# Kernel tuning notes

Measured on AMD Instinct MI355X. Metric: run time of the kernel, lower is better.

## Reference

```python
import jax, jax.numpy as jnp
import numpy as np

N_NODES = 200000
N_EDGES = 6400000


def gcn_conv(x, W, b, src, dst, n):
    """PyG GCNConv with add_self_loops=True, symmetric normalization.
    x: [n, d_in], W: [d_in, d_out], b: [d_out], src/dst: [E] int.
    """
    h = x @ W  # [n, d_out]
    # degree over graph with self-loops (edge weight 1 each, +1 self-loop)
    deg = jax.ops.segment_sum(jnp.ones(src.shape, h.dtype), dst, num_segments=n) + 1.0
    dinv = jax.lax.rsqrt(deg)  # deg >= 1, always safe
    norm = (dinv[src] * dinv[dst])[:, None]  # [E, 1]
    agg = jax.ops.segment_sum(h[src] * norm, dst, num_segments=n)  # scatter-add over targets
    agg = agg + h * (dinv * dinv)[:, None]  # self-loop term: norm_ii = dinv_i^2
    return agg + b


def setup_inputs() -> dict:
    key = jax.random.key(0)
    ks = jax.random.split(key, 8)
    x = jax.random.normal(ks[0], (N_NODES, 1), dtype=jnp.float32)
    edge_index = jax.random.randint(ks[1], (2, N_EDGES), 0, N_NODES, dtype=jnp.int64)
    # learned params (glorot-ish scale)
    W1 = jax.random.normal(ks[2], (1, 16), dtype=jnp.float32) * (1.0 / np.sqrt(1))
    b1 = jnp.zeros((16,), dtype=jnp.float32)
    W2 = jax.random.normal(ks[3], (16, 16), dtype=jnp.float32) * (1.0 / np.sqrt(16))
    b2 = jnp.zeros((16,), dtype=jnp.float32)
    Wl = jax.random.normal(ks[4], (16, 1), dtype=jnp.float32) * (1.0 / np.sqrt(16))
    bl = jnp.zeros((1,), dtype=jnp.float32)
    return {"x": x, "edge_index": edge_index, "W1": W1, "b1": b1,
            "W2": W2, "b2": b2, "Wl": Wl, "bl": bl}


def reference(x, edge_index, W1, b1, W2, b2, Wl, bl):
    src, dst = edge_index[0], edge_index[1]
    n = x.shape[0]
    h = jax.nn.relu(gcn_conv(x, W1, b1, src, dst, n))
    h = jax.nn.relu(gcn_conv(h, W2, b2, src, dst, n))
    return h @ Wl + bl  # [N, 1]
```

## Files before the change

### kernel.cpp

```cpp
#include <hip/hip_runtime.h>

#define BSHIFT 9
#define BW 512
#define BLK 512
#define BLKL 256
#define CHUNK 8192
#define BCAP 20480
#define CSR_CAP 18432

__device__ __forceinline__ int blockScanExcl512(int v, int tid, int* wsum) {
    int lane = tid & 63;
    int w = tid >> 6;
    int incl = v;
#pragma unroll
    for (int d = 1; d < 64; d <<= 1) {
        int u = __shfl_up(incl, d, 64);
        if (lane >= d) incl += u;
    }
    if (lane == 63) wsum[w] = incl;
    __syncthreads();
    if (tid < 64) {
        int x = (tid < 8) ? wsum[tid] : 0;
#pragma unroll
        for (int d = 1; d < 8; d <<= 1) {
            int u = __shfl_up(x, d, 64);
            if (lane >= d) x += u;
        }
        if (tid < 8) wsum[tid] = x;
    }
    __syncthreads();
    int base = (w == 0) ? 0 : wsum[w - 1];
    return base + incl - v;
}

__global__ __launch_bounds__(BW) void k_zero(int* __restrict__ cnt) {
    cnt[threadIdx.x] = 0;
}

__global__ __launch_bounds__(BLK) void k_bin(const int* __restrict__ src,
                                             const int* __restrict__ dst,
                                             int* __restrict__ cnt,
                                             unsigned int* __restrict__ binned, int E) {
    __shared__ int h0[BW], h1[BW];
    __shared__ int excl[BW], cur[BW], gbase[BW];
    __shared__ unsigned int vals[CHUNK];
    __shared__ unsigned short bkt[CHUNK];
    __shared__ int wsum[8];
    int t = threadIdx.x;
    int base = blockIdx.x * CHUNK;
    int cnt_e = min(CHUNK, E - base);
    h0[t] = 0; h1[t] = 0;
    __syncthreads();
    int* hr = ((t >> 6) & 1) ? h1 : h0;

    int d16[16], s16[16];
    int myBase = base + t * 16;
    int nb = 0;
    if (myBase + 16 <= E) {
        const int4* dp = (const int4*)(dst + myBase);
        const int4* sp = (const int4*)(src + myBase);
#pragma unroll
        for (int k = 0; k < 4; ++k) {
            int4 a = dp[k];
            d16[4 * k] = a.x; d16[4 * k + 1] = a.y; d16[4 * k + 2] = a.z; d16[4 * k + 3] = a.w;
            int4 c = sp[k];
            s16[4 * k] = c.x; s16[4 * k + 1] = c.y; s16[4 * k + 2] = c.z; s16[4 * k + 3] = c.w;
        }
        nb = 16;
    } else {
        for (int k = 0; k < 16; ++k) {
            int idx = myBase + k;
            if (idx < E) { d16[k] = dst[idx]; s16[k] = src[idx]; ++nb; }
        }
    }
    for (int k = 0; k < nb; ++k) atomicAdd(&hr[d16[k] >> BSHIFT], 1);
    __syncthreads();
    int hv = h0[t] + h1[t];
    int ex = blockScanExcl512(hv, t, wsum);
    excl[t] = ex;
    cur[t] = ex;
    if (hv) gbase[t] = t * BCAP + atomicAdd(&cnt[t], hv);
    __syncthreads();
    for (int k = 0; k < nb; ++k) {
        int b = d16[k] >> BSHIFT;
        int r = atomicAdd(&cur[b], 1);
        vals[r] = ((unsigned int)s16[k] << BSHIFT) | (unsigned int)(d16[k] & (BW - 1));
        bkt[r] = (unsigned short)b;
    }
    __syncthreads();
    for (int i = t; i < cnt_e; i += BLK) {
        int b = bkt[i];
        binned[gbase[b] + (i - excl[b])] = vals[i];
    }
}

__global__ __launch_bounds__(BLK) void k_csr(const unsigned int* __restrict__ binned,
                                             const int* __restrict__ cnt,
                                             const float* __restrict__ x,
                                             int* __restrict__ csrOff,
                                             int* __restrict__ deg,
                                             float* __restrict__ dinv,
                                             float* __restrict__ xd,
                                             int* __restrict__ csrSrc, int n) {
    __shared__ int dh0[BW], dh1[BW];
    __shared__ int cursor[BW];
    __shared__ int wsum[8];
    __shared__ int stage[CSR_CAP];
    int t = threadIdx.x;
    int b = blockIdx.x;
    int ebase = b * BCAP;
    int ecnt = cnt[b];
    dh0[t] = 0; dh1[t] = 0;
    __syncthreads();
    int* dh = ((t >> 6) & 1) ? dh1 : dh0;
    for (int i = t; i < ecnt; i += BLK)
        atomicAdd(&dh[binned[ebase + i] & (BW - 1)], 1);
    __syncthreads();
    int c = dh0[t] + dh1[t];
    int ex = blockScanExcl512(c, t, wsum);
    cursor[t] = ex;
    int nodeBase = b << BSHIFT;
    if (t < min(BW, n - nodeBase)) {
        int node = nodeBase + t;
        csrOff[node] = ebase + ex;
        deg[node] = c;
        float r = rsqrtf((float)(c + 1));
        dinv[node] = r;
        xd[node] = x[node] * r;
    }
    __syncthreads();
    for (int i = t; i < ecnt; i += BLK) {
        unsigned int v = binned[ebase + i];
        int r = atomicAdd(&cursor[v & (BW - 1)], 1);
        int sv = (int)(v >> BSHIFT);
        if (r < CSR_CAP) stage[r] = sv;
        else csrSrc[ebase + r] = sv;
    }
    __syncthreads();
    int m = min(ecnt, CSR_CAP);
    for (int i = t; i < m; i += BLK)
        csrSrc[ebase + i] = stage[i];
}

__global__ __launch_bounds__(BLKL) void k_l1(const int* __restrict__ csrOff,
                                             const int* __restrict__ deg,
                                             const int* __restrict__ csrSrc,
                                             const float* __restrict__ xd,
                                             const float* __restrict__ dinv,
                                             unsigned int* __restrict__ spk, int n) {
    int tid = threadIdx.x;
    int q = tid & 3;
    int node = blockIdx.x * (BLKL / 4) + (tid >> 2);
    if (node >= n) return;
    int start = csrOff[node];
    int dc = deg[node];
    float u = 0.f;
    int e = q;
    for (; e + 4 < dc; e += 8) {
        int s0 = csrSrc[start + e];
        int s1 = csrSrc[start + e + 4];
        u += xd[s0] + xd[s1];
    }
    for (; e < dc; e += 4)
        u += xd[csrSrc[start + e]];
    u += __shfl_xor(u, 1, 64);
    u += __shfl_xor(u, 2, 64);
    if (q == 0) {
        float di = dinv[node];
        float s = di * (u + xd[node]);
        unsigned int us = (__float_as_uint(s) + 0x80u) & 0xFFFFFF00u;
        unsigned int d8 = (unsigned int)min(dc, 255);
        spk[node] = us | d8;
    }
}

__global__ __launch_bounds__(BLKL) void k_l2(const int* __restrict__ csrOff,
                                             const int* __restrict__ deg,
                                             const int* __restrict__ csrSrc,
                                             const unsigned int* __restrict__ spk,
                                             const float* __restrict__ dinv,
                                             const float* __restrict__ W1,
                                             const float* __restrict__ b1,
                                             const float* __restrict__ W2,
                                             const float* __restrict__ b2,
                                             const float* __restrict__ Wl,
                                             const float* __restrict__ bl,
                                             float* __restrict__ out, int n) {
    __shared__ float sW2[256];
    __shared__ float di_tab[256];
    int tid = threadIdx.x;
    sW2[tid] = W2[tid];
    di_tab[tid] = rsqrtf((float)(tid + 1));
    int q = tid & 3;
    int node = blockIdx.x * (BLKL / 4) + (tid >> 2);

    float w1r[16], b1r[16];
#pragma unroll
    for (int j = 0; j < 16; ++j) {
        w1r[j] = W1[j];
        float bv = b1[j];
        asm volatile("" : "+v"(bv));
        b1r[j] = bv;
    }
    float4 b2q = *(const float4*)(b2 + 4 * q);
    float4 wlq = *(const float4*)(Wl + 4 * q);
    float blv = bl[0];
    __syncthreads();
    if (node >= n) return;

    int start = csrOff[node];
    int dc = deg[node];
    float G[16];
#pragma unroll
    for (int j = 0; j < 16; ++j) G[j] = 0.f;

    unsigned int uself = spk[node];
    float dself = dinv[node];
    if (q == 0) {
        float sself = __uint_as_float(uself & 0xFFFFFF00u);
#pragma unroll
        for (int j = 0; j < 16; ++j)
            G[j] = fmaf(fmaxf(fmaf(w1r[j], sself, b1r[j]), 0.f), dself, G[j]);
    }

#define EDGEACC(u, srcidx)                                                \
    {                                                                     \
        float s_ = __uint_as_float((u) & 0xFFFFFF00u);                    \
        unsigned int d8_ = (u) & 255u;                                    \
        float di_ = di_tab[d8_];                                          \
        if (__builtin_expect(d8_ == 255u, 0)) di_ = dinv[srcidx];         \
        _Pragma("unroll")                                                 \
        for (int j = 0; j < 16; ++j)                                      \
            G[j] = fmaf(fmaxf(fmaf(w1r[j], s_, b1r[j]), 0.f), di_, G[j]); \
    }

    int e = q;
    for (; e + 12 < dc; e += 16) {
        int s0 = csrSrc[start + e];
        int s1 = csrSrc[start + e + 4];
        int s2 = csrSrc[start + e + 8];
        int s3 = csrSrc[start + e + 12];
        unsigned int u0 = spk[s0];
        unsigned int u1 = spk[s1];
        unsigned int u2 = spk[s2];
        unsigned int u3 = spk[s3];
        EDGEACC(u0, s0) EDGEACC(u1, s1) EDGEACC(u2, s2) EDGEACC(u3, s3)
    }
    for (; e < dc; e += 4) {
        int s0 = csrSrc[start + e];
        unsigned int u0 = spk[s0];
        EDGEACC(u0, s0)
    }
#undef EDGEACC

#pragma unroll
    for (int j = 0; j < 16; ++j) {
        G[j] += __shfl_xor(G[j], 1, 64);
        G[j] += __shfl_xor(G[j], 2, 64);
    }

    float4 A = make_float4(0.f, 0.f, 0.f, 0.f);
#pragma unroll
    for (int j = 0; j < 16; ++j) {
        float4 w = *(const float4*)(&sW2[j * 16 + 4 * q]);
        A.x = fmaf(w.x, G[j], A.x);
        A.y = fmaf(w.y, G[j], A.y);
        A.z = fmaf(w.z, G[j], A.z);
        A.w = fmaf(w.w, G[j], A.w);
    }

    float v0 = fmaxf(fmaf(dself, A.x, b2q.x), 0.f);
    float v1 = fmaxf(fmaf(dself, A.y, b2q.y), 0.f);
    float v2 = fmaxf(fmaf(dself, A.z, b2q.z), 0.f);
    float v3 = fmaxf(fmaf(dself, A.w, b2q.w), 0.f);
    float p = fmaf(v0, wlq.x, fmaf(v1, wlq.y, fmaf(v2, wlq.z, v3 * wlq.w)));
    p += __shfl_xor(p, 1, 64);
    p += __shfl_xor(p, 2, 64);
    if (q == 0) out[node] = p + blv;
}

extern "C" void kernel_launch(void* const* d_in, const int* in_sizes, int n_in,
                              void* d_out, int out_size, void* d_ws, size_t ws_size,
                              hipStream_t stream) {
    const float* x  = (const float*)d_in[0];
    const int*   ei = (const int*)d_in[1];
    const float* W1 = (const float*)d_in[2];
    const float* b1 = (const float*)d_in[3];
    const float* W2 = (const float*)d_in[4];
    const float* b2 = (const float*)d_in[5];
    const float* Wl = (const float*)d_in[6];
    const float* bl = (const float*)d_in[7];
    float* out = (float*)d_out;

    int n = in_sizes[0];
    int E = in_sizes[1] / 2;
    const int* srcA = ei;
    const int* dstA = ei + E;
    int NB = (n + BW - 1) >> BSHIFT;

    size_t o = 0;
    auto carve = [&](size_t bytes) {
        void* p = (char*)d_ws + o;
        o = (o + bytes + 255) & ~(size_t)255;
        return p;
    };
    int* cnt          = (int*)carve(BW * 4);
    int* csrOff       = (int*)carve((size_t)n * 4);
    int* deg          = (int*)carve((size_t)n * 4);
    float* dinv       = (float*)carve((size_t)n * 4);
    float* xd         = (float*)carve((size_t)n * 4);
    unsigned int* spk = (unsigned int*)carve((size_t)n * 4);
    unsigned int* binned = (unsigned int*)carve((size_t)NB * BCAP * 4);
    int* csrSrc       = (int*)carve((size_t)NB * BCAP * 4);
    (void)ws_size;

    k_zero<<<1, BW, 0, stream>>>(cnt);
    k_bin<<<(E + CHUNK - 1) / CHUNK, BLK, 0, stream>>>(srcA, dstA, cnt, binned, E);
    k_csr<<<NB, BLK, 0, stream>>>(binned, cnt, x, csrOff, deg, dinv, xd, csrSrc, n);

    int nodeBlocks = (n + (BLKL / 4) - 1) / (BLKL / 4);
    k_l1<<<nodeBlocks, BLKL, 0, stream>>>(csrOff, deg, csrSrc, xd, dinv, spk, n);
    k_l2<<<nodeBlocks, BLKL, 0, stream>>>(csrOff, deg, csrSrc, spk, dinv,
                                          W1, b1, W2, b2, Wl, bl, out, n);
}
```

Measured before the change: 132.5 us.

## Pre-gather packed source values into padded CSR before layer-2 aggregation

k_csr now pads each node's CSR segment to a multiple of 4 and zero-fills the padding, with the row lengths recorded per bin. A new k_gather kernel then overwrites each source index in place with that source's packed scale+degree word. This lets k_l2 read edge values with aligned uint4 loads instead of a dependent index-then-random-gather chain. In exchange there is an extra kernel launch and an extra read and write pass over the CSR. The layer-2 path also drops the exact dinv fallback for sources with degree at or above 255, so such nodes would get a wrong normalisation.

```diff
diff --git a/kernel.cpp b/kernel.cpp
--- a/kernel.cpp
+++ b/kernel.cpp
@@ -101,10 +101,12 @@
                                              int* __restrict__ deg,
                                              float* __restrict__ dinv,
                                              float* __restrict__ xd,
-                                             int* __restrict__ csrSrc, int n) {
+                                             int* __restrict__ padcnt,
+                                             int* __restrict__ csr, int n) {
     __shared__ int dh0[BW], dh1[BW];
     __shared__ int cursor[BW];
     __shared__ int wsum[8];
+    __shared__ int padtot_s;
     __shared__ int stage[CSR_CAP];
     int t = threadIdx.x;
     int b = blockIdx.x;
@@ -117,8 +119,10 @@
         atomicAdd(&dh[binned[ebase + i] & (BW - 1)], 1);
     __syncthreads();
     int c = dh0[t] + dh1[t];
-    int ex = blockScanExcl512(c, t, wsum);
+    int pad4 = (c + 3) & ~3;
+    int ex = blockScanExcl512(pad4, t, wsum);
     cursor[t] = ex;
+    if (t == BLK - 1) padtot_s = ex + pad4;
     int nodeBase = b << BSHIFT;
     if (t < min(BW, n - nodeBase)) {
         int node = nodeBase + t;
@@ -129,22 +133,30 @@
         xd[node] = x[node] * r;
     }
     __syncthreads();
+    int padtot = padtot_s;
+    int mcap = min(padtot, CSR_CAP);
+    int4* st4 = (int4*)stage;
+    int4 z4 = make_int4(0, 0, 0, 0);
+    for (int i = t; i < (mcap >> 2); i += BLK) st4[i] = z4;
+    for (int i = CSR_CAP + t; i < padtot; i += BLK) csr[ebase + i] = 0;
+    __syncthreads();
     for (int i = t; i < ecnt; i += BLK) {
         unsigned int v = binned[ebase + i];
         int r = atomicAdd(&cursor[v & (BW - 1)], 1);
         int sv = (int)(v >> BSHIFT);
         if (r < CSR_CAP) stage[r] = sv;
-        else csrSrc[ebase + r] = sv;
-    }
-    __syncthreads();
-    int m = min(ecnt, CSR_CAP);
-    for (int i = t; i < m; i += BLK)
-        csrSrc[ebase + i] = stage[i];
+        else csr[ebase + r] = sv;
+    }
+    __syncthreads();
+    int4* out4 = (int4*)(csr + ebase);
+    for (int i = t; i < (mcap >> 2); i += BLK)
+        out4[i] = st4[i];
+    if (t == 0) padcnt[b] = padtot;
 }
 
 __global__ __launch_bounds__(BLKL) void k_l1(const int* __restrict__ csrOff,
                                              const int* __restrict__ deg,
-                                             const int* __restrict__ csrSrc,
+                                             const int* __restrict__ csr,
                                              const float* __restrict__ xd,
                                              const float* __restrict__ dinv,
                                              unsigned int* __restrict__ spk, int n) {
@@ -157,12 +169,12 @@
     float u = 0.f;
     int e = q;
     for (; e + 4 < dc; e += 8) {
-        int s0 = csrSrc[start + e];
-        int s1 = csrSrc[start + e + 4];
+        int s0 = csr[start + e];
+        int s1 = csr[start + e + 4];
         u += xd[s0] + xd[s1];
     }
     for (; e < dc; e += 4)
-        u += xd[csrSrc[start + e]];
+        u += xd[csr[start + e]];
     u += __shfl_xor(u, 1, 64);
     u += __shfl_xor(u, 2, 64);
     if (q == 0) {
@@ -174,9 +186,29 @@
     }
 }
 
+__global__ __launch_bounds__(BLK) void k_gather(const int* __restrict__ padcnt,
+                                                const unsigned int* __restrict__ spk,
+                                                unsigned int* __restrict__ csr) {
+    int t = threadIdx.x;
+    int b = blockIdx.x;
+    unsigned int* base = csr + (size_t)b * BCAP;
+    int len = padcnt[b];
+    for (int i = t * 8; i + 8 <= len; i += BLK * 8) {
+        int4 a = *(const int4*)(base + i);
+        int4 c = *(const int4*)(base + i + 4);
+        unsigned int v0 = spk[a.x], v1 = spk[a.y], v2 = spk[a.z], v3 = spk[a.w];
+        unsigned int v4 = spk[c.x], v5 = spk[c.y], v6 = spk[c.z], v7 = spk[c.w];
+        *(uint4*)(base + i) = make_uint4(v0, v1, v2, v3);
+        *(uint4*)(base + i + 4) = make_uint4(v4, v5, v6, v7);
+    }
+    int tail = len & ~7;
+    for (int i = tail + t; i < len; i += BLK)
+        base[i] = spk[base[i]];
+}
+
 __global__ __launch_bounds__(BLKL) void k_l2(const int* __restrict__ csrOff,
                                              const int* __restrict__ deg,
-                                             const int* __restrict__ csrSrc,
+                                             const unsigned int* __restrict__ csrVal,
                                              const unsigned int* __restrict__ spk,
                                              const float* __restrict__ dinv,
                                              const float* __restrict__ W1,
@@ -223,35 +255,25 @@
             G[j] = fmaf(fmaxf(fmaf(w1r[j], sself, b1r[j]), 0.f), dself, G[j]);
     }
 
-#define EDGEACC(u, srcidx)                                                \
+#define VALACC(u)                                                         \
     {                                                                     \
         float s_ = __uint_as_float((u) & 0xFFFFFF00u);                    \
-        unsigned int d8_ = (u) & 255u;                                    \
-        float di_ = di_tab[d8_];                                          \
-        if (__builtin_expect(d8_ == 255u, 0)) di_ = dinv[srcidx];         \
+        float di_ = di_tab[(u) & 255u];                                   \
         _Pragma("unroll")                                                 \
         for (int j = 0; j < 16; ++j)                                      \
             G[j] = fmaf(fmaxf(fmaf(w1r[j], s_, b1r[j]), 0.f), di_, G[j]); \
     }
 
-    int e = q;
-    for (; e + 12 < dc; e += 16) {
-        int s0 = csrSrc[start + e];
-        int s1 = csrSrc[start + e + 4];
-        int s2 = csrSrc[start + e + 8];
-        int s3 = csrSrc[start + e + 12];
-        unsigned int u0 = spk[s0];
-        unsigned int u1 = spk[s1];
-        unsigned int u2 = spk[s2];
-        unsigned int u3 = spk[s3];
-        EDGEACC(u0, s0) EDGEACC(u1, s1) EDGEACC(u2, s2) EDGEACC(u3, s3)
-    }
-    for (; e < dc; e += 4) {
-        int s0 = csrSrc[start + e];
-        unsigned int u0 = spk[s0];
-        EDGEACC(u0, s0)
-    }
-#undef EDGEACC
+    int pos = 0;
+    for (; pos + 16 <= dc; pos += 16) {
+        uint4 u = *(const uint4*)(csrVal + start + pos + q * 4);
+        VALACC(u.x) VALACC(u.y) VALACC(u.z) VALACC(u.w)
+    }
+    for (int e = pos + q; e < dc; e += 4) {
+        unsigned int u = csrVal[start + e];
+        VALACC(u)
+    }
+#undef VALACC
 
 #pragma unroll
     for (int j = 0; j < 16; ++j) {
@@ -305,21 +327,23 @@
         return p;
     };
     int* cnt          = (int*)carve(BW * 4);
+    int* padcnt       = (int*)carve(BW * 4);
     int* csrOff       = (int*)carve((size_t)n * 4);
     int* deg          = (int*)carve((size_t)n * 4);
     float* dinv       = (float*)carve((size_t)n * 4);
     float* xd         = (float*)carve((size_t)n * 4);
     unsigned int* spk = (unsigned int*)carve((size_t)n * 4);
     unsigned int* binned = (unsigned int*)carve((size_t)NB * BCAP * 4);
-    int* csrSrc       = (int*)carve((size_t)NB * BCAP * 4);
+    int* csr          = (int*)carve((size_t)NB * BCAP * 4);
     (void)ws_size;
 
     k_zero<<<1, BW, 0, stream>>>(cnt);
     k_bin<<<(E + CHUNK - 1) / CHUNK, BLK, 0, stream>>>(srcA, dstA, cnt, binned, E);
-    k_csr<<<NB, BLK, 0, stream>>>(binned, cnt, x, csrOff, deg, dinv, xd, csrSrc, n);
+    k_csr<<<NB, BLK, 0, stream>>>(binned, cnt, x, csrOff, deg, dinv, xd, padcnt, csr, n);
 
     int nodeBlocks = (n + (BLKL / 4) - 1) / (BLKL / 4);
-    k_l1<<<nodeBlocks, BLKL, 0, stream>>>(csrOff, deg, csrSrc, xd, dinv, spk, n);
-    k_l2<<<nodeBlocks, BLKL, 0, stream>>>(csrOff, deg, csrSrc, spk, dinv,
+    k_l1<<<nodeBlocks, BLKL, 0, stream>>>(csrOff, deg, csr, xd, dinv, spk, n);
+    k_gather<<<NB, BLK, 0, stream>>>(padcnt, spk, (unsigned int*)csr);
+    k_l2<<<nodeBlocks, BLKL, 0, stream>>>(csrOff, deg, (unsigned int*)csr, spk, dinv,
                                           W1, b1, W2, b2, Wl, bl, out, n);
 }
```

Measured after the change: 151.8 us. 14.6% more time.
